# Kernel optimization log

Measured on AMD Instinct MI355X. Metric: run time of the kernel, lower is better.

The kernel has to match this reference:

```python
import jax, jax.numpy as jnp
import numpy as np

DIM = 1024      # feature_size
K = 128         # num_clusters
E = 2           # expansion
G = 8           # groups
ITERN = 3       # Newton-Schulz iterations
DG = E * DIM // G  # 256 per-group dim


def setup_inputs() -> dict:
    key = jax.random.key(0)
    ks = jax.random.split(key, 10)
    f32 = jnp.float32
    return {
        "x": jax.random.normal(ks[0], (32, DIM, 16, 8), dtype=f32),
        "centroids": jax.random.normal(ks[1], (K, DG), dtype=f32) * 0.05,
        "W_inp": jax.random.normal(ks[2], (E * DIM, DIM), dtype=f32) * 0.02,
        "b_inp": jax.random.normal(ks[3], (E * DIM,), dtype=f32) * 0.01,
        "W_g": jax.random.normal(ks[4], (G, E * DIM), dtype=f32) * 0.02,
        "b_g": jax.random.normal(ks[5], (G,), dtype=f32) * 0.01,
        "W_gk": jax.random.normal(ks[6], (G * K, E * DIM), dtype=f32) * 0.02,
        "b_gk": jax.random.normal(ks[7], (G * K,), dtype=f32) * 0.01,
        "W_f": jax.random.normal(ks[8], (1, K), dtype=f32) * 0.05,
        "b_f": jax.random.normal(ks[9], (1,), dtype=f32) * 0.01,
    }


def _covpool(v):
    # v: [bs, d, h, w] -> second-order pooling [bs, d, d]; x @ I_hat @ x^T == centered outer product / M
    bs, d = v.shape[0], v.shape[1]
    m = v.shape[2] * v.shape[3]
    v = v.reshape(bs, d, m)
    vc = v - v.mean(axis=2, keepdims=True)
    return jnp.einsum('bdm,bem->bde', vc, vc) / m


def _sqrtm_ns(cov, iter_n):
    # MPNCOV Newton-Schulz matrix square root (iter_n >= 2)
    d = cov.shape[1]
    I3 = 3.0 * jnp.eye(d, dtype=cov.dtype)[None]
    norm_a = jnp.trace(cov, axis1=1, axis2=2)[:, None, None]  # pre-normalization by trace
    A = cov / norm_a
    ZY = 0.5 * (I3 - A)
    Y = A @ ZY
    Z = ZY
    for _ in range(1, iter_n - 1):
        ZY = 0.5 * (I3 - Z @ Y)
        Y, Z = Y @ ZY, ZY @ Z
    ZY = 0.5 * (Y @ (I3 - Z @ Y))
    return ZY * jnp.sqrt(norm_a)


def _triuvec(cov):
    # row-major upper-triangular (incl. diagonal) vectorization, matching MPNCOV Triuvec
    d = cov.shape[1]
    r, c = np.triu_indices(d)
    return cov[:, r, c]


def reference(x, centroids, W_inp, b_inp, W_g, b_g, W_gk, b_gk, W_f, b_f):
    resolution = x.shape[-1]
    b8, C, H, W = x.shape
    bs = b8 // 8
    # [bs*8, C, H, W] -> [bs, M, N] with M = 8*H*W, N = C
    xt = x.reshape(bs, 8, C, H, W).transpose(0, 2, 1, 3, 4).reshape(bs, C, 8 * H * W)
    xt = jnp.transpose(xt, (0, 2, 1))
    M = xt.shape[1]
    # L2-normalize along feature dim (F.normalize eps clamp)
    xt = xt / jnp.maximum(jnp.linalg.norm(xt, axis=2, keepdims=True), 1e-12)
    h = xt @ W_inp.T + b_inp                               # [bs, M, E*N]
    alpha_g = jax.nn.sigmoid(h @ W_g.T + b_g)              # [bs, M, G]
    alpha_gk = jax.nn.softmax(h @ W_gk.T + b_gk, axis=1)   # NOTE: nn.Softmax(dim=1) -> over M
    alpha_gk = alpha_gk.reshape(bs, M, G, K)
    rx = h.reshape(bs, M, G, DG)                           # [bs, M, G, DG]
    w = alpha_g[..., None] * alpha_gk                      # [bs, M, G, K]
    # fused residual-weighted sum over M: sum_m w*(x - c) = (sum_m w*x) - (sum_m w)*c
    vlad = jnp.einsum('bmgk,bmgd->bgkd', w, rx) - w.sum(axis=1)[..., None] * centroids
    # learnable fusion over clusters K
    vf = jnp.einsum('bgkd,k->bgd', vlad, W_f[0]) + b_f[0]  # [bs, G, DG]
    vf = jnp.transpose(vf, (0, 2, 1))                      # [bs, DG, G]
    vf = vf.reshape(bs, DG, G // resolution, resolution)
    cov = _covpool(vf)
    cov = _sqrtm_ns(cov, ITERN)
    return _triuvec(cov)                                   # [bs, DG*(DG+1)//2]
```

## Files before the change

### kernel.cpp

```cpp
#include <hip/hip_runtime.h>
#include <math.h>

typedef float f32x4 __attribute__((ext_vector_type(4)));
typedef short bf16x8 __attribute__((ext_vector_type(8)));
typedef unsigned short u16;

__device__ __forceinline__ u16 f2bf(float f) {
    unsigned u = __builtin_bit_cast(unsigned, f);
    u += 0x7fff + ((u >> 16) & 1);
    return (u16)(u >> 16);
}
__device__ __forceinline__ float bf2f(u16 s) {
    unsigned v = ((unsigned)s) << 16;
    return __builtin_bit_cast(float, v);
}
__device__ __forceinline__ void gload16(const void* g, void* l) {
    __builtin_amdgcn_global_load_lds(
        (const __attribute__((address_space(1))) unsigned int*)g,
        (__attribute__((address_space(3))) unsigned int*)l, 16, 0, 0);
}

__global__ __launch_bounds__(256) void k_pre(const float* __restrict__ x,
                                             const float* __restrict__ Wgk,
                                             const float* __restrict__ Winp,
                                             const float* __restrict__ Wg,
                                             const float* __restrict__ binp,
                                             const float* __restrict__ bg,
                                             u16* __restrict__ xtn,
                                             u16* __restrict__ wgkb,
                                             u16* __restrict__ winpT,
                                             float* __restrict__ wge,
                                             float* __restrict__ cg) {
    int bid = blockIdx.x, tid = threadIdx.x;
    if (bid < 512) {
        int b8 = bid >> 4, hh = bid & 15;
        __shared__ float tile[8][1032];
        __shared__ float inv[8];
        const float* src = x + (size_t)b8 * 1024 * 128 + hh * 8;
        #pragma unroll
        for (int r = 0; r < 4; ++r) {
            int c = tid * 4 + r;
            const float* p = src + (size_t)c * 128;
            float4 v0 = *(const float4*)(p);
            float4 v1 = *(const float4*)(p + 4);
            tile[0][c] = v0.x; tile[1][c] = v0.y; tile[2][c] = v0.z; tile[3][c] = v0.w;
            tile[4][c] = v1.x; tile[5][c] = v1.y; tile[6][c] = v1.z; tile[7][c] = v1.w;
        }
        __syncthreads();
        int w = tid >> 5, j = tid & 31;
        float s = 0.f;
        #pragma unroll 8
        for (int i = 0; i < 32; ++i) { float v = tile[w][i * 32 + j]; s += v * v; }
        #pragma unroll
        for (int m = 16; m; m >>= 1) s += __shfl_xor(s, m);
        if (j == 0) inv[w] = 1.0f / fmaxf(sqrtf(s), 1e-12f);
        __syncthreads();
        int b = b8 >> 3, t = b8 & 7;
        int c0 = tid * 4;
        for (int w2 = 0; w2 < 8; ++w2) {
            int m = t * 128 + hh * 8 + w2;
            float sc = inv[w2];
            u16* dst = xtn + ((size_t)b * 1024 + m) * 1024;
            ushort4 o;
            o.x = f2bf(tile[w2][c0 + 0] * sc);
            o.y = f2bf(tile[w2][c0 + 1] * sc);
            o.z = f2bf(tile[w2][c0 + 2] * sc);
            o.w = f2bf(tile[w2][c0 + 3] * sc);
            *(ushort4*)(dst + c0) = o;
        }
    } else if (bid < 2560) {
        int i = ((bid - 512) * 256 + tid) * 4;
        float4 v = *(const float4*)(Wgk + i);
        ushort4 o;
        o.x = f2bf(v.x); o.y = f2bf(v.y); o.z = f2bf(v.z); o.w = f2bf(v.w);
        *(ushort4*)(wgkb + i) = o;
    } else if (bid < 3072) {
        int tb = bid - 2560;
        int er = tb & 31, cr = tb >> 5;
        __shared__ float tile[64][65];
        #pragma unroll
        for (int i = 0; i < 16; ++i) {
            int idx = tid + i * 256;
            int r = idx >> 6, c = idx & 63;
            tile[r][c] = Winp[(size_t)(er * 64 + r) * 1024 + cr * 64 + c];
        }
        __syncthreads();
        #pragma unroll
        for (int i = 0; i < 16; ++i) {
            int idx = tid + i * 256;
            int cc = idx >> 6, rr = idx & 63;
            winpT[(size_t)(cr * 64 + cc) * 2048 + er * 64 + rr] = f2bf(tile[rr][cc]);
        }
    } else {
        int t2 = bid - 3072;
        int cs = t2 & 3, es = t2 >> 2;
        __shared__ float wg_l[8][64];
        #pragma unroll
        for (int i = 0; i < 2; ++i) {
            int idx = tid + i * 256;
            wg_l[idx >> 6][idx & 63] = Wg[(size_t)(idx >> 6) * 2048 + es * 64 + (idx & 63)];
        }
        __syncthreads();
        int c = cs * 256 + tid;
        float acc[8] = {};
        #pragma unroll 4
        for (int e = 0; e < 64; ++e) {
            float v = Winp[(size_t)(es * 64 + e) * 1024 + c];
            #pragma unroll
            for (int g = 0; g < 8; ++g) acc[g] += wg_l[g][e] * v;
        }
        #pragma unroll
        for (int g = 0; g < 8; ++g) atomicAdd(&wge[g * 1024 + c], acc[g]);
        if (cs == 0) {
            int g = tid >> 5, sub = tid & 31;
            float t = 0.f;
            for (int e = sub; e < 64; e += 32) t += wg_l[g][e] * binp[es * 64 + e];
            #pragma unroll
            for (int m = 16; m; m >>= 1) t += __shfl_xor(t, m);
            if (sub == 0) {
                if (es == 0) t += bg[g];
                atomicAdd(&cg[g], t);
            }
        }
    }
}

template <int MODE>
__global__ __launch_bounds__(256, 4) void k_mfma_gemm(
    const u16* __restrict__ A, const u16* __restrict__ B,
    float* __restrict__ Cf, u16* __restrict__ Cb,
    const float* __restrict__ agT, float* __restrict__ ssum, float* __restrict__ sagm,
    int Kld, int Kloop, int N,
    long long zA, long long zB, long long zC)
{
    constexpr int MR = 2, NR = 2;
    __shared__ u16 As[2][64 * 64];
    __shared__ u16 Bs[2][64 * 64];
    int bz = blockIdx.z;
    A += (size_t)bz * zA; B += (size_t)bz * zB;
    int tid = threadIdx.x, lane = tid & 63, wave = tid >> 6;
    int wr = wave >> 1, wc = wave & 1;
    int i0 = blockIdx.y * 64, j0 = blockIdx.x * 64;
    int fr = lane & 15, fg = lane >> 4;
    f32x4 acc[MR][NR] = {};

    int srcOff = ((tid & 7) ^ ((tid >> 3) & 7)) * 8;
    int srow = tid >> 3;

    auto stage = [&](int buf, int t) {
        int kt = t * 64;
        #pragma unroll
        for (int q = 0; q < 2; ++q)
            gload16(A + (size_t)(i0 + q * 32 + srow) * Kld + kt + srcOff,
                    &As[buf][(q * 256 + wave * 64) * 8]);
        #pragma unroll
        for (int q = 0; q < 2; ++q)
            gload16(B + (size_t)(j0 + q * 32 + srow) * Kld + kt + srcOff,
                    &Bs[buf][(q * 256 + wave * 64) * 8]);
    };
    auto compute = [&](int buf) {
        #pragma unroll
        for (int h = 0; h < 2; ++h) {
            bf16x8 af[MR], bv[NR];
            #pragma unroll
            for (int mi = 0; mi < MR; ++mi) {
                int row = wr * 32 + mi * 16 + fr;
                af[mi] = *(const bf16x8*)&As[buf][row * 64 + (((h * 4 + fg) ^ (fr & 7)) * 8)];
            }
            #pragma unroll
            for (int ni = 0; ni < NR; ++ni) {
                int row = wc * 32 + ni * 16 + fr;
                bv[ni] = *(const bf16x8*)&Bs[buf][row * 64 + (((h * 4 + fg) ^ (fr & 7)) * 8)];
            }
            #pragma unroll
            for (int mi = 0; mi < MR; ++mi)
                #pragma unroll
                for (int ni = 0; ni < NR; ++ni)
                    acc[mi][ni] = __builtin_amdgcn_mfma_f32_16x16x32_bf16(
                        af[mi], bv[ni], acc[mi][ni], 0, 0, 0);
        }
    };

    int nk = Kloop >> 6;
    stage(0, 0);
    int cur = 0;
    for (int t = 0; t < nk; ++t) {
        if (t + 1 < nk) {
            stage(cur ^ 1, t + 1);
            asm volatile("s_waitcnt vmcnt(4)" ::: "memory");
        } else {
            asm volatile("s_waitcnt vmcnt(0)" ::: "memory");
        }
        __builtin_amdgcn_s_barrier();
        __builtin_amdgcn_sched_barrier(0);
        compute(cur);
        __builtin_amdgcn_s_barrier();
        cur ^= 1;
    }

    if constexpr (MODE == 3) {
        int bcol = j0 >> 10;
        float ag2[NR];
        #pragma unroll
        for (int ni = 0; ni < NR; ++ni) {
            int col = j0 + wc * 32 + ni * 16 + fr;
            int g = i0 >> 7;
            ag2[ni] = agT[((size_t)bcol * 8 + g) * 1024 + (col & 1023)];
        }
        #pragma unroll
        for (int mi = 0; mi < MR; ++mi)
            #pragma unroll
            for (int r = 0; r < 4; ++r) {
                int row = i0 + wr * 32 + mi * 16 + fg * 4 + r;
                float es = 0.f, sa = 0.f;
                #pragma unroll
                for (int ni = 0; ni < NR; ++ni) {
                    int col = j0 + wc * 32 + ni * 16 + fr;
                    float e = expf(acc[mi][ni][r]);
                    es += e; sa += ag2[ni] * e;
                    Cb[(size_t)row * N + col] = f2bf(e - 1.f);
                }
                #pragma unroll
                for (int m = 8; m; m >>= 1) { es += __shfl_xor(es, m); sa += __shfl_xor(sa, m); }
                if (fr == 0) {
                    atomicAdd(&ssum[row * 4 + bcol], es);
                    atomicAdd(&sagm[row * 4 + bcol], sa);
                }
            }
    } else {
        float* C2 = Cf + (size_t)bz * zC;
        #pragma unroll
        for (int ni = 0; ni < NR; ++ni) {
            int col = j0 + wc * 32 + ni * 16 + fr;
            #pragma unroll
            for (int mi = 0; mi < MR; ++mi)
                #pragma unroll
                for (int r = 0; r < 4; ++r) {
                    int row = i0 + wr * 32 + mi * 16 + fg * 4 + r;
                    C2[(size_t)row * N + col] = acc[mi][ni][r];
                }
        }
    }
}

__global__ __launch_bounds__(256) void k_mid(const float* __restrict__ wcp,
                                             u16* __restrict__ wcb,
                                             const u16* __restrict__ xtn,
                                             const float* __restrict__ wge,
                                             const float* __restrict__ cg,
                                             float* __restrict__ agT) {
    int bid = blockIdx.x, tid = threadIdx.x;
    if (bid < 1024) {
        int i = (bid * 256 + tid) * 4;
        float4 a = *(const float4*)(wcp + i);
        float4 b = *(const float4*)(wcp + 1048576 + i);
        float4 c = *(const float4*)(wcp + 2097152 + i);
        float4 d = *(const float4*)(wcp + 3145728 + i);
        ushort4 o;
        o.x = f2bf(a.x + b.x + c.x + d.x);
        o.y = f2bf(a.y + b.y + c.y + d.y);
        o.z = f2bf(a.z + b.z + c.z + d.z);
        o.w = f2bf(a.w + b.w + c.w + d.w);
        *(ushort4*)(wcb + i) = o;
    } else {
        int t2 = bid - 1024;
        int b = t2 >> 5, ms = t2 & 31;
        int w = tid >> 6, lane = tid & 63;
        __shared__ float wgel[8192];
        __shared__ float cgl[8];
        #pragma unroll
        for (int i = 0; i < 8; ++i) {
            int idx = tid + i * 256;
            *(float4*)&wgel[idx * 4] = *(const float4*)&wge[idx * 4];
        }
        if (tid < 8) cgl[tid] = cg[tid];
        __syncthreads();
        for (int r = 0; r < 8; ++r) {
            int m = ms * 32 + w * 8 + r;
            const u16* xr = xtn + ((size_t)b * 1024 + m) * 1024;
            float acc[8] = {};
            #pragma unroll
            for (int i = 0; i < 2; ++i) {
                int c0 = i * 512 + lane * 8;
                bf16x8 hv = *(const bf16x8*)(xr + c0);
                float xf[8];
                #pragma unroll
                for (int j = 0; j < 8; ++j) xf[j] = bf2f((u16)hv[j]);
                #pragma unroll
                for (int g = 0; g < 8; ++g) {
                    float4 wa = *(const float4*)&wgel[g * 1024 + c0];
                    float4 wb = *(const float4*)&wgel[g * 1024 + c0 + 4];
                    acc[g] += xf[0] * wa.x + xf[1] * wa.y + xf[2] * wa.z + xf[3] * wa.w
                            + xf[4] * wb.x + xf[5] * wb.y + xf[6] * wb.z + xf[7] * wb.w;
                }
            }
            #pragma unroll
            for (int g = 0; g < 8; ++g)
                #pragma unroll
                for (int off = 32; off; off >>= 1) acc[g] += __shfl_xor(acc[g], off);
            if (lane < 8)
                agT[((size_t)b * 8 + lane) * 1024 + m] =
                    1.f / (1.f + expf(-(acc[lane] + cgl[lane])));
        }
    }
}

__global__ __launch_bounds__(256) void k_wf2(const u16* __restrict__ em1,
                                             const float* __restrict__ ssum,
                                             const float* __restrict__ sagm,
                                             const float* __restrict__ Wf,
                                             const float* __restrict__ agT,
                                             float* __restrict__ wf, float* __restrict__ u) {
    int ms = blockIdx.x, bg = blockIdx.y;
    int b = bg >> 3, g = bg & 7;
    int tid = threadIdx.x;
    __shared__ float c1[128];
    __shared__ float part[256];
    __shared__ float c0s;
    if (tid < 128) {
        int gk = g * 128 + tid;
        float s = ssum[gk * 4 + b];
        float wfk = Wf[tid];
        float cv = wfk / s;
        c1[tid] = cv;
        part[tid] = cv;
        if (ms == 0) u[bg * 128 + tid] = wfk * sagm[gk * 4 + b] / s;
    } else part[tid] = 0.f;
    __syncthreads();
    for (int st = 128; st; st >>= 1) { if (tid < st) part[tid] += part[tid + st]; __syncthreads(); }
    if (tid == 0) c0s = part[0];
    __syncthreads();
    float C0 = c0s;
    int ml = tid & 127, kh = tid >> 7;
    const u16* base = em1 + (size_t)(g * 128 + kh * 64) * 4096 + b * 1024 + ms * 128;
    float acc = 0.f;
    #pragma unroll 4
    for (int k = 0; k < 64; ++k)
        acc += c1[kh * 64 + k] * bf2f(base[(size_t)k * 4096 + ml]);
    __syncthreads();
    part[tid] = acc;
    __syncthreads();
    if (tid < 128) {
        float agv = agT[((size_t)b * 8 + g) * 1024 + ms * 128 + tid];
        wf[(size_t)bg * 1024 + ms * 128 + tid] = (C0 + part[tid] + part[tid + 128]) * agv;
    }
}

__global__ __launch_bounds__(256) void k_wfx(const u16* __restrict__ xtn,
                                             const float* __restrict__ wf,
                                             float* __restrict__ wfxp) {
    int cs = blockIdx.x, ms = blockIdx.y, b = blockIdx.z;
    int tid = threadIdx.x;
    __shared__ float wfl[8][128];
    #pragma unroll
    for (int i = 0; i < 4; ++i) {
        int idx = tid + i * 256;
        wfl[idx >> 7][idx & 127] = wf[((size_t)b * 8 + (idx >> 7)) * 1024 + ms * 128 + (idx & 127)];
    }
    __syncthreads();
    int c = cs * 256 + tid;
    float acc[8] = {};
    for (int m = 0; m < 128; ++m) {
        float xv = bf2f(xtn[((size_t)b * 1024 + ms * 128 + m) * 1024 + c]);
        #pragma unroll
        for (int g = 0; g < 8; ++g) acc[g] += wfl[g][m] * xv;
    }
    #pragma unroll
    for (int g = 0; g < 8; ++g)
        wfxp[(((size_t)ms * 4 + b) * 8 + g) * 1024 + c] = acc[g];
}

__global__ __launch_bounds__(256) void k_vfpart(const float* __restrict__ wfxp,
                                                const u16* __restrict__ winpT,
                                                const float* __restrict__ u,
                                                const float* __restrict__ cent,
                                                const float* __restrict__ binp,
                                                float* __restrict__ vfp) {
    int g = blockIdx.x, cs = blockIdx.y;
    int tid = threadIdx.x;
    if (cs < 8) {
        __shared__ float wfx_l[4][128];
        #pragma unroll
        for (int i = 0; i < 2; ++i) {
            int idx = tid + i * 256;
            int bb = idx >> 7, c2 = idx & 127;
            float s = 0.f;
            #pragma unroll
            for (int msq = 0; msq < 8; ++msq)
                s += wfxp[(((size_t)msq * 4 + bb) * 8 + g) * 1024 + cs * 128 + c2];
            wfx_l[bb][c2] = s;
        }
        __syncthreads();
        int d = tid;
        float acc[4] = {};
        for (int c2 = 0; c2 < 128; ++c2) {
            float wv = bf2f(winpT[(size_t)(cs * 128 + c2) * 2048 + g * 256 + d]);
            #pragma unroll
            for (int bb = 0; bb < 4; ++bb) acc[bb] += wfx_l[bb][c2] * wv;
        }
        #pragma unroll
        for (int bb = 0; bb < 4; ++bb)
            vfp[(((size_t)bb * 8 + g) * 9 + cs) * 256 + d] = acc[bb];
    } else {
        __shared__ float ul[4][128];
        __shared__ float swl[4];
        #pragma unroll
        for (int i = 0; i < 2; ++i) {
            int idx = tid + i * 256;
            ul[idx >> 7][idx & 127] = u[((size_t)(idx >> 7) * 8 + g) * 128 + (idx & 127)];
        }
        __syncthreads();
        if (tid < 4) {
            float s = 0.f;
            for (int k = 0; k < 128; ++k) s += ul[tid][k];
            swl[tid] = s;
        }
        __syncthreads();
        int d = tid;
        float acc[4] = {};
        for (int k = 0; k < 128; ++k) {
            float cv = cent[k * 256 + d];
            #pragma unroll
            for (int bb = 0; bb < 4; ++bb) acc[bb] -= ul[bb][k] * cv;
        }
        float bi = binp[g * 256 + d];
        #pragma unroll
        for (int bb = 0; bb < 4; ++bb)
            vfp[(((size_t)bb * 8 + g) * 9 + 8) * 256 + d] = acc[bb] + swl[bb] * bi;
    }
}

#define MM8(DST, P, Q) do { if (act) { float s_ = 0.f; \
    _Pragma("unroll") \
    for (int l_ = 0; l_ < 8; ++l_) s_ += P[ii][l_] * Q[l_][jj]; \
    DST[ii][jj] = s_; } __syncthreads(); } while (0)

__global__ __launch_bounds__(256) void k_fin(const float* __restrict__ vfp,
                                             const float* __restrict__ bf,
                                             float* __restrict__ out) {
    int b = blockIdx.x;
    int tid = threadIdx.x, d = tid;
    __shared__ float Vl[256][9];
    __shared__ float4 Vl4a[256], Vl4b[256];
    __shared__ float red[256];
    __shared__ float Sp[4][64];
    __shared__ float Sm[8][8], W1[8][8], W2[8][8], YmL[8][8], ZmL[8][8], ZYL[8][8], FmL[8][8];
    float bfv = bf[0];
    float vfl[8];
    #pragma unroll
    for (int g = 0; g < 8; ++g) {
        float acc = 0.f;
        for (int mc = 0; mc < 9; ++mc)
            acc += vfp[(((size_t)b * 8 + g) * 9 + mc) * 256 + d];
        vfl[g] = acc + bfv;
    }
    float mean = 0.f;
    #pragma unroll
    for (int g = 0; g < 8; ++g) mean += vfl[g];
    mean *= 0.125f;
    float trp = 0.f;
    #pragma unroll
    for (int g = 0; g < 8; ++g) { float v = vfl[g] - mean; Vl[d][g] = v; vfl[g] = v; trp += v * v; }
    Vl4a[d] = make_float4(vfl[0], vfl[1], vfl[2], vfl[3]);
    Vl4b[d] = make_float4(vfl[4], vfl[5], vfl[6], vfl[7]);
    red[tid] = trp;
    __syncthreads();
    for (int s = 128; s > 0; s >>= 1) { if (tid < s) red[tid] += red[tid + s]; __syncthreads(); }
    float tr = red[0] * 0.125f;
    {
        int q = tid >> 6, l = tid & 63;
        int si = l >> 3, sj = l & 7;
        float sv = 0.f;
        for (int dd = q * 64; dd < q * 64 + 64; ++dd) sv += Vl[dd][si] * Vl[dd][sj];
        Sp[q][l] = sv;
    }
    __syncthreads();
    bool act = tid < 64;
    int ii = (tid >> 3) & 7, jj = tid & 7;
    if (act) Sm[ii][jj] = (Sp[0][tid] + Sp[1][tid] + Sp[2][tid] + Sp[3][tid]) / (8.f * tr);
    __syncthreads();
    if (act) {
        YmL[ii][jj] = (ii == jj ? 1.5f : 0.f) - 0.5f * Sm[ii][jj];
        ZmL[ii][jj] = (ii == jj ? -0.5f : 0.f);
    }
    __syncthreads();
    float ya = 0.f, za = 1.5f;
    MM8(W1, Sm, YmL);
    MM8(W2, ZmL, W1);
    float pa = za * ya;
    if (act) ZYL[ii][jj] = -0.5f * (za * YmL[ii][jj] + ya * ZmL[ii][jj] + W2[ii][jj]);
    __syncthreads();
    float zya = 1.5f - 0.5f * pa;
    MM8(W1, Sm, ZYL);
    MM8(W2, YmL, W1);
    if (act) YmL[ii][jj] = ya * ZYL[ii][jj] + zya * YmL[ii][jj] + W2[ii][jj];
    __syncthreads();
    ya = ya * zya;
    MM8(W1, Sm, ZmL);
    MM8(W2, ZYL, W1);
    if (act) ZmL[ii][jj] = zya * ZmL[ii][jj] + za * ZYL[ii][jj] + W2[ii][jj];
    __syncthreads();
    za = zya * za;
    MM8(W1, Sm, YmL);
    MM8(W2, ZmL, W1);
    float p2a = za * ya;
    if (act) ZYL[ii][jj] = za * YmL[ii][jj] + ya * ZmL[ii][jj] + W2[ii][jj];
    __syncthreads();
    MM8(W1, Sm, ZYL);
    MM8(W2, YmL, W1);
    if (act) FmL[ii][jj] = 0.5f * ((3.f - p2a) * YmL[ii][jj] - ya * ZYL[ii][jj] - W2[ii][jj]);
    __syncthreads();
    float fa = 0.5f * ya * (3.f - p2a);
    float sqtr = sqrtf(tr);
    float scaleF = 1.f / (8.f * sqtr);
    float wrj[8];
    #pragma unroll
    for (int jo = 0; jo < 8; ++jo) {
        float sv = 0.f;
        #pragma unroll
        for (int i = 0; i < 8; ++i) sv += vfl[i] * FmL[i][jo];
        wrj[jo] = sv * scaleF;
    }
    float s0v = fa * sqtr;
    size_t base = (size_t)b * 32896 + (size_t)d * 256 - ((size_t)d * (d - 1)) / 2 - d;
    for (int e = d; e < 256; ++e) {
        float4 va = Vl4a[e], vb = Vl4b[e];
        float v = wrj[0] * va.x + wrj[1] * va.y + wrj[2] * va.z + wrj[3] * va.w
                + wrj[4] * vb.x + wrj[5] * vb.y + wrj[6] * vb.z + wrj[7] * vb.w;
        if (e == d) v += s0v;
        out[base + e] = v;
    }
}

extern "C" void kernel_launch(void* const* d_in, const int* in_sizes, int n_in,
                              void* d_out, int out_size, void* d_ws, size_t ws_size,
                              hipStream_t stream) {
    const float* x    = (const float*)d_in[0];
    const float* cent = (const float*)d_in[1];
    const float* Winp = (const float*)d_in[2];
    const float* binp = (const float*)d_in[3];
    const float* Wg   = (const float*)d_in[4];
    const float* bg   = (const float*)d_in[5];
    const float* Wgk  = (const float*)d_in[6];
    const float* Wf   = (const float*)d_in[8];
    const float* bf   = (const float*)d_in[9];
    float* out = (float*)d_out;
    char* wsb = (char*)d_ws;

    u16*   xtnb  = (u16*)(wsb);
    u16*   ltb   = (u16*)(wsb + (8ull << 20));
    u16*   wgkb  = (u16*)(wsb + (16ull << 20));
    u16*   winpT = (u16*)(wsb + (20ull << 20));
    float* wcp   = (float*)(wsb + (24ull << 20));
    u16*   wcb   = (u16*)(wsb + (40ull << 20));
    float* misc  = (float*)(wsb + (42ull << 20));
    float* wge   = misc;
    float* cg    = wge + 8192;
    float* ssum  = cg + 8;
    float* sagm  = ssum + 4096;
    float* agT   = sagm + 4096;
    float* u     = agT + 32768;
    float* wf    = u + 4096;
    float* wfxp  = wf + 32768;
    float* vfp   = wfxp + 262144;

    hipMemsetAsync(misc, 0, 16392 * sizeof(float), stream);
    k_pre<<<3200, 256, 0, stream>>>(x, Wgk, Winp, Wg, binp, bg, xtnb, wgkb, winpT, wge, cg);
    k_mfma_gemm<0><<<dim3(16, 16, 4), 256, 0, stream>>>(
        wgkb, winpT, wcp, nullptr, nullptr, nullptr, nullptr,
        2048, 512, 1024, 512LL, 512LL, 1048576LL);
    k_mid<<<1152, 256, 0, stream>>>(wcp, wcb, xtnb, wge, cg, agT);
    k_mfma_gemm<3><<<dim3(64, 16, 1), 256, 0, stream>>>(
        wcb, xtnb, nullptr, ltb, agT, ssum, sagm,
        1024, 1024, 4096, 0, 0, 0);
    k_wf2<<<dim3(8, 32), 256, 0, stream>>>(ltb, ssum, sagm, Wf, agT, wf, u);
    k_wfx<<<dim3(4, 8, 4), 256, 0, stream>>>(xtnb, wf, wfxp);
    k_vfpart<<<dim3(8, 9), 256, 0, stream>>>(wfxp, winpT, u, cent, binp, vfp);
    k_fin<<<4, 256, 0, stream>>>(vfp, bf, out);
}
```

Before: 145.3 us.

## Drop memset and atomics, fuse wf kernels, parallelize final triuvec output

Replaces the atomic accumulation of W_g·W_inp with per-slice partial buffers that k_mid reduces, and computes the g-bias in one block. The separate memset becomes a zeroing block inside k_mid. The two wf kernels are merged into one that builds wf in shared memory and applies it to xtn directly. k_fin is split across 8 row-slices per batch so the triangular output is written by more blocks with coalesced stores. Each slice redundantly recomputes the 8x8 Newton-Schulz chain, and the fused kernel launches only 64 blocks.

```diff
diff --git a/kernel.cpp b/kernel.cpp
--- a/kernel.cpp
+++ b/kernel.cpp
@@ -29,7 +29,7 @@
                                              u16* __restrict__ xtn,
                                              u16* __restrict__ wgkb,
                                              u16* __restrict__ winpT,
-                                             float* __restrict__ wge,
+                                             float* __restrict__ wgp,
                                              float* __restrict__ cg) {
     int bid = blockIdx.x, tid = threadIdx.x;
     if (bid < 512) {
@@ -91,37 +91,32 @@
             int cc = idx >> 6, rr = idx & 63;
             winpT[(size_t)(cr * 64 + cc) * 2048 + er * 64 + rr] = f2bf(tile[rr][cc]);
         }
+    } else if (bid < 3088) {
+        int t2 = bid - 3072;
+        int cq = t2 & 3, eq = t2 >> 2;
+        __shared__ float wg_l[8][512];
+        #pragma unroll
+        for (int i = 0; i < 16; ++i) {
+            int idx = tid + i * 256;
+            wg_l[idx >> 9][idx & 511] = Wg[(size_t)(idx >> 9) * 2048 + eq * 512 + (idx & 511)];
+        }
+        __syncthreads();
+        int c = cq * 256 + tid;
+        float acc[8] = {};
+        for (int e = 0; e < 512; ++e) {
+            float v = Winp[(size_t)(eq * 512 + e) * 1024 + c];
+            #pragma unroll
+            for (int g = 0; g < 8; ++g) acc[g] += wg_l[g][e] * v;
+        }
+        #pragma unroll
+        for (int g = 0; g < 8; ++g) wgp[(size_t)eq * 8192 + g * 1024 + c] = acc[g];
     } else {
-        int t2 = bid - 3072;
-        int cs = t2 & 3, es = t2 >> 2;
-        __shared__ float wg_l[8][64];
-        #pragma unroll
-        for (int i = 0; i < 2; ++i) {
-            int idx = tid + i * 256;
-            wg_l[idx >> 6][idx & 63] = Wg[(size_t)(idx >> 6) * 2048 + es * 64 + (idx & 63)];
-        }
-        __syncthreads();
-        int c = cs * 256 + tid;
-        float acc[8] = {};
-        #pragma unroll 4
-        for (int e = 0; e < 64; ++e) {
-            float v = Winp[(size_t)(es * 64 + e) * 1024 + c];
-            #pragma unroll
-            for (int g = 0; g < 8; ++g) acc[g] += wg_l[g][e] * v;
-        }
-        #pragma unroll
-        for (int g = 0; g < 8; ++g) atomicAdd(&wge[g * 1024 + c], acc[g]);
-        if (cs == 0) {
-            int g = tid >> 5, sub = tid & 31;
-            float t = 0.f;
-            for (int e = sub; e < 64; e += 32) t += wg_l[g][e] * binp[es * 64 + e];
-            #pragma unroll
-            for (int m = 16; m; m >>= 1) t += __shfl_xor(t, m);
-            if (sub == 0) {
-                if (es == 0) t += bg[g];
-                atomicAdd(&cg[g], t);
-            }
-        }
+        int g = tid >> 5, sub = tid & 31;
+        float t = 0.f;
+        for (int e = sub; e < 2048; e += 32) t += Wg[(size_t)g * 2048 + e] * binp[e];
+        #pragma unroll
+        for (int m = 16; m; m >>= 1) t += __shfl_xor(t, m);
+        if (sub == 0) cg[g] = t + bg[g];
     }
 }
 
@@ -200,11 +195,11 @@
 
     if constexpr (MODE == 3) {
         int bcol = j0 >> 10;
+        int g = i0 >> 7;
         float ag2[NR];
         #pragma unroll
         for (int ni = 0; ni < NR; ++ni) {
             int col = j0 + wc * 32 + ni * 16 + fr;
-            int g = i0 >> 7;
             ag2[ni] = agT[((size_t)bcol * 8 + g) * 1024 + (col & 1023)];
         }
         #pragma unroll
@@ -246,9 +241,10 @@
 __global__ __launch_bounds__(256) void k_mid(const float* __restrict__ wcp,
                                              u16* __restrict__ wcb,
                                              const u16* __restrict__ xtn,
-                                             const float* __restrict__ wge,
+                                             const float* __restrict__ wgp,
                                              const float* __restrict__ cg,
-                                             float* __restrict__ agT) {
+                                             float* __restrict__ agT,
+                                             float* __restrict__ zz) {
     int bid = blockIdx.x, tid = threadIdx.x;
     if (bid < 1024) {
         int i = (bid * 256 + tid) * 4;
@@ -262,7 +258,7 @@
         o.z = f2bf(a.z + b.z + c.z + d.z);
         o.w = f2bf(a.w + b.w + c.w + d.w);
         *(ushort4*)(wcb + i) = o;
-    } else {
+    } else if (bid < 1152) {
         int t2 = bid - 1024;
         int b = t2 >> 5, ms = t2 & 31;
         int w = tid >> 6, lane = tid & 63;
@@ -270,8 +266,17 @@
         __shared__ float cgl[8];
         #pragma unroll
         for (int i = 0; i < 8; ++i) {
-            int idx = tid + i * 256;
-            *(float4*)&wgel[idx * 4] = *(const float4*)&wge[idx * 4];
+            int idx = (tid + i * 256) * 4;
+            float4 p0 = *(const float4*)&wgp[idx];
+            float4 p1 = *(const float4*)&wgp[8192 + idx];
+            float4 p2 = *(const float4*)&wgp[16384 + idx];
+            float4 p3 = *(const float4*)&wgp[24576 + idx];
+            float4 s;
+            s.x = p0.x + p1.x + p2.x + p3.x;
+            s.y = p0.y + p1.y + p2.y + p3.y;
+            s.z = p0.z + p1.z + p2.z + p3.z;
+            s.w = p0.w + p1.w + p2.w + p3.w;
+            *(float4*)&wgel[idx] = s;
         }
         if (tid < 8) cgl[tid] = cg[tid];
         __syncthreads();
@@ -302,72 +307,76 @@
                 agT[((size_t)b * 8 + lane) * 1024 + m] =
                     1.f / (1.f + expf(-(acc[lane] + cgl[lane])));
         }
-    }
-}
-
-__global__ __launch_bounds__(256) void k_wf2(const u16* __restrict__ em1,
-                                             const float* __restrict__ ssum,
-                                             const float* __restrict__ sagm,
-                                             const float* __restrict__ Wf,
-                                             const float* __restrict__ agT,
-                                             float* __restrict__ wf, float* __restrict__ u) {
-    int ms = blockIdx.x, bg = blockIdx.y;
-    int b = bg >> 3, g = bg & 7;
+    } else {
+        float4 z = make_float4(0.f, 0.f, 0.f, 0.f);
+        #pragma unroll
+        for (int i = 0; i < 8; ++i)
+            *(float4*)&zz[(tid + i * 256) * 4] = z;
+    }
+}
+
+__global__ __launch_bounds__(256) void k_wfx2(const u16* __restrict__ em1,
+                                              const float* __restrict__ ssum,
+                                              const float* __restrict__ sagm,
+                                              const float* __restrict__ Wf,
+                                              const float* __restrict__ agT,
+                                              const u16* __restrict__ xtn,
+                                              float* __restrict__ wfxp,
+                                              float* __restrict__ u) {
+    int ms = blockIdx.x, b = blockIdx.y, gh = blockIdx.z;
     int tid = threadIdx.x;
-    __shared__ float c1[128];
-    __shared__ float part[256];
-    __shared__ float c0s;
-    if (tid < 128) {
-        int gk = g * 128 + tid;
-        float s = ssum[gk * 4 + b];
-        float wfk = Wf[tid];
-        float cv = wfk / s;
-        c1[tid] = cv;
-        part[tid] = cv;
-        if (ms == 0) u[bg * 128 + tid] = wfk * sagm[gk * 4 + b] / s;
-    } else part[tid] = 0.f;
-    __syncthreads();
-    for (int st = 128; st; st >>= 1) { if (tid < st) part[tid] += part[tid + st]; __syncthreads(); }
-    if (tid == 0) c0s = part[0];
-    __syncthreads();
-    float C0 = c0s;
-    int ml = tid & 127, kh = tid >> 7;
-    const u16* base = em1 + (size_t)(g * 128 + kh * 64) * 4096 + b * 1024 + ms * 128;
-    float acc = 0.f;
-    #pragma unroll 4
-    for (int k = 0; k < 64; ++k)
-        acc += c1[kh * 64 + k] * bf2f(base[(size_t)k * 4096 + ml]);
-    __syncthreads();
-    part[tid] = acc;
-    __syncthreads();
-    if (tid < 128) {
-        float agv = agT[((size_t)b * 8 + g) * 1024 + ms * 128 + tid];
-        wf[(size_t)bg * 1024 + ms * 128 + tid] = (C0 + part[tid] + part[tid + 128]) * agv;
-    }
-}
-
-__global__ __launch_bounds__(256) void k_wfx(const u16* __restrict__ xtn,
-                                             const float* __restrict__ wf,
-                                             float* __restrict__ wfxp) {
-    int cs = blockIdx.x, ms = blockIdx.y, b = blockIdx.z;
-    int tid = threadIdx.x;
-    __shared__ float wfl[8][128];
+    int g0 = gh * 4;
+    __shared__ float c1[512];
+    __shared__ float C0[4];
+    __shared__ float wf_l[4][128];
     #pragma unroll
-    for (int i = 0; i < 4; ++i) {
-        int idx = tid + i * 256;
-        wfl[idx >> 7][idx & 127] = wf[((size_t)b * 8 + (idx >> 7)) * 1024 + ms * 128 + (idx & 127)];
-    }
-    __syncthreads();
-    int c = cs * 256 + tid;
-    float acc[8] = {};
-    for (int m = 0; m < 128; ++m) {
-        float xv = bf2f(xtn[((size_t)b * 1024 + ms * 128 + m) * 1024 + c]);
-        #pragma unroll
-        for (int g = 0; g < 8; ++g) acc[g] += wfl[g][m] * xv;
-    }
+    for (int i = 0; i < 2; ++i) {
+        int kk = tid + i * 256;
+        int gk = g0 * 128 + kk;
+        float cv = Wf[gk & 127] / ssum[gk * 4 + b];
+        c1[kk] = cv;
+        if (ms == 0) u[(size_t)b * 1024 + gk] = cv * sagm[gk * 4 + b];
+    }
+    __syncthreads();
+    {
+        int w = tid >> 6, l = tid & 63;
+        float s = c1[w * 128 + l] + c1[w * 128 + 64 + l];
+        #pragma unroll
+        for (int m = 32; m; m >>= 1) s += __shfl_xor(s, m);
+        if (l == 0) C0[w] = s;
+    }
+    __syncthreads();
+    {
+        int w = tid >> 6, l = tid & 63;
+        int g = g0 + w;
+        float a0 = 0.f, a1 = 0.f;
+        const u16* base = em1 + (size_t)(g * 128) * 4096 + b * 1024 + ms * 128 + 2 * l;
+        for (int k = 0; k < 128; ++k) {
+            unsigned pr = *(const unsigned*)(base + (size_t)k * 4096);
+            float cv = c1[w * 128 + k];
+            a0 += cv * bf2f((u16)(pr & 0xffff));
+            a1 += cv * bf2f((u16)(pr >> 16));
+        }
+        float c0v = C0[w];
+        const float* agp = agT + ((size_t)b * 8 + g) * 1024 + ms * 128;
+        wf_l[w][2 * l]     = (c0v + a0) * agp[2 * l];
+        wf_l[w][2 * l + 1] = (c0v + a1) * agp[2 * l + 1];
+    }
+    __syncthreads();
     #pragma unroll
-    for (int g = 0; g < 8; ++g)
-        wfxp[(((size_t)ms * 4 + b) * 8 + g) * 1024 + c] = acc[g];
+    for (int cs = 0; cs < 4; ++cs) {
+        int c = cs * 256 + tid;
+        float acc[4] = {};
+        const u16* xb = xtn + ((size_t)b * 1024 + ms * 128) * 1024 + c;
+        for (int m = 0; m < 128; ++m) {
+            float xv = bf2f(xb[(size_t)m * 1024]);
+            #pragma unroll
+            for (int lg = 0; lg < 4; ++lg) acc[lg] += wf_l[lg][m] * xv;
+        }
+        #pragma unroll
+        for (int lg = 0; lg < 4; ++lg)
+            wfxp[(((size_t)ms * 4 + b) * 8 + g0 + lg) * 1024 + c] = acc[lg];
+    }
 }
 
 __global__ __launch_bounds__(256) void k_vfpart(const float* __restrict__ wfxp,
@@ -438,10 +447,11 @@
 __global__ __launch_bounds__(256) void k_fin(const float* __restrict__ vfp,
                                              const float* __restrict__ bf,
                                              float* __restrict__ out) {
-    int b = blockIdx.x;
+    int slice = blockIdx.x, b = blockIdx.y;
     int tid = threadIdx.x, d = tid;
     __shared__ float Vl[256][9];
     __shared__ float4 Vl4a[256], Vl4b[256];
+    __shared__ float Wr_l[256][8];
     __shared__ float red[256];
     __shared__ float Sp[4][64];
     __shared__ float Sm[8][8], W1[8][8], W2[8][8], YmL[8][8], ZmL[8][8], ZYL[8][8], FmL[8][8];
@@ -513,22 +523,28 @@
     float fa = 0.5f * ya * (3.f - p2a);
     float sqtr = sqrtf(tr);
     float scaleF = 1.f / (8.f * sqtr);
-    float wrj[8];
     #pragma unroll
     for (int jo = 0; jo < 8; ++jo) {
         float sv = 0.f;
         #pragma unroll
         for (int i = 0; i < 8; ++i) sv += vfl[i] * FmL[i][jo];
-        wrj[jo] = sv * scaleF;
+        Wr_l[d][jo] = sv * scaleF;
     }
     float s0v = fa * sqtr;
-    size_t base = (size_t)b * 32896 + (size_t)d * 256 - ((size_t)d * (d - 1)) / 2 - d;
-    for (int e = d; e < 256; ++e) {
-        float4 va = Vl4a[e], vb = Vl4b[e];
-        float v = wrj[0] * va.x + wrj[1] * va.y + wrj[2] * va.z + wrj[3] * va.w
-                + wrj[4] * vb.x + wrj[5] * vb.y + wrj[6] * vb.z + wrj[7] * vb.w;
-        if (e == d) v += s0v;
-        out[base + e] = v;
+    __syncthreads();
+    int dd0 = slice * 32;
+    for (int dd = dd0; dd < dd0 + 32; ++dd) {
+        int e = tid;
+        if (e >= dd) {
+            float w0 = Wr_l[dd][0], w1 = Wr_l[dd][1], w2 = Wr_l[dd][2], w3 = Wr_l[dd][3];
+            float w4 = Wr_l[dd][4], w5 = Wr_l[dd][5], w6 = Wr_l[dd][6], w7 = Wr_l[dd][7];
+            float4 va = Vl4a[e], vb = Vl4b[e];
+            float v = w0 * va.x + w1 * va.y + w2 * va.z + w3 * va.w
+                    + w4 * vb.x + w5 * vb.y + w6 * vb.z + w7 * vb.w;
+            if (e == dd) v += s0v;
+            size_t base = (size_t)b * 32896 + (size_t)dd * 256 - ((size_t)dd * (dd - 1)) / 2;
+            out[base + (e - dd)] = v;
+        }
     }
 }
 
@@ -554,27 +570,24 @@
     float* wcp   = (float*)(wsb + (24ull << 20));
     u16*   wcb   = (u16*)(wsb + (40ull << 20));
     float* misc  = (float*)(wsb + (42ull << 20));
-    float* wge   = misc;
-    float* cg    = wge + 8192;
+    float* wgp   = misc;
+    float* cg    = wgp + 32768;
     float* ssum  = cg + 8;
     float* sagm  = ssum + 4096;
     float* agT   = sagm + 4096;
     float* u     = agT + 32768;
-    float* wf    = u + 4096;
-    float* wfxp  = wf + 32768;
+    float* wfxp  = u + 4096;
     float* vfp   = wfxp + 262144;
 
-    hipMemsetAsync(misc, 0, 16392 * sizeof(float), stream);
-    k_pre<<<3200, 256, 0, stream>>>(x, Wgk, Winp, Wg, binp, bg, xtnb, wgkb, winpT, wge, cg);
+    k_pre<<<3089, 256, 0, stream>>>(x, Wgk, Winp, Wg, binp, bg, xtnb, wgkb, winpT, wgp, cg);
     k_mfma_gemm<0><<<dim3(16, 16, 4), 256, 0, stream>>>(
         wgkb, winpT, wcp, nullptr, nullptr, nullptr, nullptr,
         2048, 512, 1024, 512LL, 512LL, 1048576LL);
-    k_mid<<<1152, 256, 0, stream>>>(wcp, wcb, xtnb, wge, cg, agT);
+    k_mid<<<1153, 256, 0, stream>>>(wcp, wcb, xtnb, wgp, cg, agT, ssum);
     k_mfma_gemm<3><<<dim3(64, 16, 1), 256, 0, stream>>>(
         wcb, xtnb, nullptr, ltb, agT, ssum, sagm,
         1024, 1024, 4096, 0, 0, 0);
-    k_wf2<<<dim3(8, 32), 256, 0, stream>>>(ltb, ssum, sagm, Wf, agT, wf, u);
-    k_wfx<<<dim3(4, 8, 4), 256, 0, stream>>>(xtnb, wf, wfxp);
+    k_wfx2<<<dim3(8, 4, 2), 256, 0, stream>>>(ltb, ssum, sagm, Wf, agT, xtnb, wfxp, u);
     k_vfpart<<<dim3(8, 9), 256, 0, stream>>>(wfxp, winpT, u, cent, binp, vfp);
-    k_fin<<<4, 256, 0, stream>>>(vfp, bf, out);
-}
+    k_fin<<<dim3(8, 4), 256, 0, stream>>>(vfp, bf, out);
+}
```

Result: slower. 193.3 us (+33.1%).
